# Kernel optimization log

Hardware: AMD Instinct MI355X
Metric: run time of the kernel (lower is better)

The kernel has to match this reference:

```python
import jax, jax.numpy as jnp
import numpy as np

NS, NV = 32, 8                      # scalar / vector multiplicities (32x0e + 8x1o)
N_NODES, N_EDGES = 16384, 131072
NEF, HID = 128, 128                 # edge feature dim, MLP hidden
WN = NS*NS + NV*NS + NS*NV + NV*NV  # 1600 tensor-product weights per edge
D = NS + 3*NV                       # 56 node feature dim
INV_SQRT3 = 1.0/np.sqrt(3.0)        # CG coeff for 1o x 1o -> 0e
PATH_NORM = 1.0/np.sqrt(NS + NV)    # fan-in normalization per output irrep
EPS = 1e-5


def setup_inputs() -> dict:
    key = jax.random.key(0)
    ks = jax.random.split(key, 10)
    node_attr = jax.random.normal(ks[0], (N_NODES, D), jnp.float32)
    edge_index = jax.random.randint(ks[1], (2, N_EDGES), 0, N_NODES, dtype=jnp.int64)
    edge_attr = jax.random.normal(ks[2], (N_EDGES, NEF), jnp.float32)
    edge_sh = jax.random.normal(ks[3], (N_EDGES, 4), jnp.float32)
    W1 = jax.random.normal(ks[4], (NEF, HID), jnp.float32) / np.sqrt(NEF)
    b1 = jnp.zeros((HID,), jnp.float32)
    W2 = jax.random.normal(ks[5], (HID, WN), jnp.float32) / np.sqrt(HID)
    b2 = jnp.zeros((WN,), jnp.float32)
    bn_gamma = jnp.ones((NS + NV,), jnp.float32)   # per-irrep scale (scalars then vectors)
    bn_beta = jnp.zeros((NS,), jnp.float32)        # bias only on scalar irreps
    return dict(node_attr=node_attr, edge_attr=edge_attr, edge_sh=edge_sh,
                W1=W1, b1=b1, W2=W2, b2=b2, bn_gamma=bn_gamma, bn_beta=bn_beta,
                edge_index=edge_index)


def reference(node_attr, edge_attr, edge_sh, W1, b1, W2, b2, bn_gamma, bn_beta, edge_index):
    edge_src, edge_dst = edge_index[0], edge_index[1]

    # per-edge tensor-product weights from edge MLP (dropout=0, eval mode)
    w = jax.nn.relu(edge_attr @ W1 + b1) @ W2 + b2            # [E, WN]
    o0 = NS*NS; o1 = o0 + NV*NS; o2 = o1 + NS*NV
    w_ss = w[:, :o0].reshape(-1, NS, NS)   # 0e x 0e -> 0e
    w_vs = w[:, o0:o1].reshape(-1, NV, NS) # 1o x 1o -> 0e
    w_sv = w[:, o1:o2].reshape(-1, NS, NV) # 0e x 1o -> 1o
    w_vv = w[:, o2:].reshape(-1, NV, NV)   # 1o x 0e -> 1o

    # gather node features onto edges
    x = node_attr[edge_dst]                # [E, D]
    xs = x[:, :NS]                         # [E, NS]
    xv = x[:, NS:].reshape(-1, NV, 3)      # [E, NV, 3]
    ss = edge_sh[:, 0]                     # [E]
    sv = edge_sh[:, 1:4]                   # [E, 3]

    # CG tensor product with per-edge fully-connected weights
    dot_vv = jnp.einsum('eim,em->ei', xv, sv) * INV_SQRT3
    out_s = (jnp.einsum('eij,ei->ej', w_ss, xs) * ss[:, None]
             + jnp.einsum('eij,ei->ej', w_vs, dot_vv)) * PATH_NORM          # [E, NS]
    out_v = (jnp.einsum('eij,ei->ej', w_sv, xs)[:, :, None] * sv[:, None, :]
             + jnp.einsum('eij,eim->ejm', w_vv, xv) * ss[:, None, None]) * PATH_NORM  # [E, NV, 3]
    tp = jnp.concatenate([out_s, out_v.reshape(-1, 3*NV)], axis=-1)         # [E, D]

    # scatter-mean to source nodes
    sums = jax.ops.segment_sum(tp, edge_src, num_segments=N_NODES)
    cnt = jax.ops.segment_sum(jnp.ones((tp.shape[0], 1), tp.dtype), edge_src,
                              num_segments=N_NODES)
    out = sums / jnp.maximum(cnt, 1.0)

    # residual (in/out irreps identical -> zero padding is a no-op)
    out = out + node_attr

    # equivariant batch norm (training-mode batch statistics)
    s = out[:, :NS]
    v = out[:, NS:].reshape(-1, NV, 3)
    s = (s - s.mean(0)) / jnp.sqrt(s.var(0) + EPS) * bn_gamma[:NS] + bn_beta
    vn2 = (v * v).sum(-1).mean(0)                               # [NV] mean squared norm
    v = v / jnp.sqrt(vn2 + EPS)[None, :, None] * bn_gamma[NS:][None, :, None]
    return jnp.concatenate([s, v.reshape(-1, 3*NV)], axis=-1)
```

## Files before the change

### kernel.cpp

```cpp
#include <hip/hip_runtime.h>

typedef short short8 __attribute__((ext_vector_type(8)));
typedef unsigned short us4 __attribute__((ext_vector_type(4)));
typedef float floatx4 __attribute__((ext_vector_type(4)));
typedef unsigned short u16;

#define NN 16384
#define NE 131072
#define NEF_ 128
#define DD 56
#define INV_SQRT3F 0.57735026918962576f
#define PATH_NORMF 0.15811388300841897f

__device__ __forceinline__ float bf2f(u16 u) {
    union { unsigned int i; float f; } v; v.i = ((unsigned int)u) << 16; return v.f;
}
__device__ __forceinline__ u16 f2bf(float f) {
    union { float f; unsigned int i; } v; v.f = f;
    unsigned int r = v.i + 0x7fffu + ((v.i >> 16) & 1u);
    return (u16)(r >> 16);
}

__global__ __launch_bounds__(256) void prep(const float* __restrict__ W1,
                                            const float* __restrict__ W2,
                                            u16* __restrict__ W1T,
                                            u16* __restrict__ W2T,
                                            const int* __restrict__ eidx,
                                            int* __restrict__ deg) {
    int b = blockIdx.x;
    if (b < 864) {
        int i = b * 256 + threadIdx.x;
        if (i < 16384) {
            int n = i >> 7, k = i & 127;
            W1T[i] = f2bf(W1[k * 128 + n]);
        } else {
            int j = i - 16384;
            int n = j >> 7, k = j & 127;
            W2T[j] = f2bf(W2[k * 1600 + n]);
        }
    } else {
        int e = (b - 864) * 256 + threadIdx.x;
        atomicAdd(&deg[eidx[e]], 1);
    }
}

__global__ __launch_bounds__(1024) void deg_scan(const int* __restrict__ deg,
                                                 int* __restrict__ row_start,
                                                 int* __restrict__ cursor) {
    __shared__ int part[1024];
    const int t = threadIdx.x;
    const int base = t * 16;
    int loc[16];
    int s = 0;
    #pragma unroll
    for (int i = 0; i < 16; i++) { loc[i] = s; s += deg[base + i]; }
    part[t] = s;
    __syncthreads();
    for (int off = 1; off < 1024; off <<= 1) {
        int v = (t >= off) ? part[t - off] : 0;
        __syncthreads();
        part[t] += v;
        __syncthreads();
    }
    int pre = (t == 0) ? 0 : part[t - 1];
    #pragma unroll
    for (int i = 0; i < 16; i++) {
        int v = pre + loc[i];
        row_start[base + i] = v;
        cursor[base + i] = v;
    }
    if (t == 1023) row_start[16384] = pre + s;
}

__global__ __launch_bounds__(256) void edge_scatter(const int* __restrict__ eidx,
                                                    int* __restrict__ cursor,
                                                    int* __restrict__ edge_order) {
    int e = blockIdx.x * 256 + threadIdx.x;
    int p = atomicAdd(&cursor[eidx[e]], 1);
    edge_order[p] = e;
}

__global__ __launch_bounds__(512, 4) void tpconv(
    const float* __restrict__ node_attr, const float* __restrict__ edge_attr,
    const float* __restrict__ edge_sh, const u16* __restrict__ W1T,
    const float* __restrict__ b1, const u16* __restrict__ W2T,
    const float* __restrict__ b2, const int* __restrict__ eidx,
    const int* __restrict__ edge_order,
    float* __restrict__ tp)
{
    __shared__ __align__(16) char smem[49920];
    u16*   sA  = (u16*)smem;
    u16*   sB  = (u16*)(smem + 17408);
    u16*   sF  = (u16*)(smem + 34816);
    float* b2s = (float*)(smem + 43520);
    float* Ssc  = (float*)smem;
    float* Svec = (float*)(smem + 16896);

    const int t = threadIdx.x;
    const int lane = t & 63;
    const int wv = t >> 6;
    const int m = lane & 15;
    const int q = lane >> 4;
    const int cg = wv & 3;
    const int eh = wv >> 2;
    const int eb = eh * 32;
    const int p0 = blockIdx.x * 64;
    const int str = t >> 4;
    const int stc = (t & 15) * 8;

    short8 pre[2];
    #pragma unroll
    for (int ii = 0; ii < 2; ii++)
        pre[ii] = *(const short8*)&W2T[(size_t)(str + 32 * ii) * 128 + stc];

    for (int i = t; i < 1600; i += 512) b2s[i] = b2[i];

    #pragma unroll
    for (int ii = 0; ii < 4; ii++) {
        int cid = t + 512 * ii;
        int r = cid >> 5, s = cid & 31;
        int e = edge_order[p0 + r];
        const float* src = &edge_attr[(size_t)e * NEF_ + s * 4];
        us4 o;
        o.x = f2bf(src[0]); o.y = f2bf(src[1]); o.z = f2bf(src[2]); o.w = f2bf(src[3]);
        *(us4*)&sA[r * 136 + s * 4] = o;
    }
    if (t < 64) {
        int e = edge_order[p0 + t];
        int nd = eidx[NE + e];
        const float* na = node_attr + (size_t)nd * DD;
        const float* sh = edge_sh + (size_t)e * 4;
        float ss = sh[0], s0 = sh[1], s1 = sh[2], s2 = sh[3];
        #pragma unroll
        for (int i = 0; i < 32; i++) sF[i * 64 + t] = f2bf(na[i]);
        #pragma unroll
        for (int i = 0; i < 8; i++) {
            float d = (na[32+i*3]*s0 + na[33+i*3]*s1 + na[34+i*3]*s2) * INV_SQRT3F;
            sF[(32 + i) * 64 + t] = f2bf(d);
        }
        #pragma unroll
        for (int i = 0; i < 24; i++) sF[(40 + i) * 64 + t] = f2bf(na[32 + i]);
        sF[64 * 64 + t] = f2bf(ss);
        sF[65 * 64 + t] = f2bf(s0);
        sF[66 * 64 + t] = f2bf(s1);
        sF[67 * 64 + t] = f2bf(s2);
    }
    __syncthreads();

    floatx4 hacc[2][2];
    #pragma unroll
    for (int cc = 0; cc < 2; cc++) {
        #pragma unroll
        for (int ii = 0; ii < 2; ii++)
            *(short8*)&sB[(str + 32 * ii) * 136 + stc] =
                *(const short8*)&W1T[(size_t)(cc * 64 + str + 32 * ii) * 128 + stc];
        __syncthreads();
        {
            float bv = b1[cc * 64 + cg * 16 + m];
            hacc[cc][0] = (floatx4){bv, bv, bv, bv};
            hacc[cc][1] = hacc[cc][0];
        }
        #pragma unroll
        for (int k0 = 0; k0 < 128; k0 += 32) {
            short8 a0 = *(const short8*)&sA[(eb      + m) * 136 + k0 + q * 8];
            short8 a1 = *(const short8*)&sA[(eb + 16 + m) * 136 + k0 + q * 8];
            short8 bA = *(const short8*)&sB[(cg * 16 + m) * 136 + k0 + q * 8];
            hacc[cc][0] = __builtin_amdgcn_mfma_f32_16x16x32_bf16(a0, bA, hacc[cc][0], 0, 0, 0);
            hacc[cc][1] = __builtin_amdgcn_mfma_f32_16x16x32_bf16(a1, bA, hacc[cc][1], 0, 0, 0);
        }
        __syncthreads();
    }
    #pragma unroll
    for (int cc = 0; cc < 2; cc++)
      #pragma unroll
      for (int rt = 0; rt < 2; rt++)
        #pragma unroll
        for (int r = 0; r < 4; r++) {
            int e   = eb + rt * 16 + q * 4 + r;
            int col = cc * 64 + cg * 16 + m;
            float v = hacc[cc][rt][r];
            sA[e * 136 + col] = f2bf(v > 0.f ? v : 0.f);
        }
    __syncthreads();

    short8 hc[2][4];
    #pragma unroll
    for (int et = 0; et < 2; et++)
        #pragma unroll
        for (int kk = 0; kk < 4; kk++)
            hc[et][kk] = *(const short8*)&sA[(eb + et * 16 + m) * 136 + kk * 32 + q * 8];

    float ssc[2], svc[2][3];
    #pragma unroll
    for (int et = 0; et < 2; et++) {
        ssc[et] = bf2f(sF[64 * 64 + eb + et * 16 + m]);
        svc[et][0] = bf2f(sF[65 * 64 + eb + et * 16 + m]);
        svc[et][1] = bf2f(sF[66 * 64 + eb + et * 16 + m]);
        svc[et][2] = bf2f(sF[67 * 64 + eb + et * 16 + m]);
    }

    #pragma unroll
    for (int ii = 0; ii < 2; ii++)
        *(short8*)&sB[(str + 32 * ii) * 136 + stc] = pre[ii];
    #pragma unroll
    for (int ii = 0; ii < 2; ii++)
        pre[ii] = *(const short8*)&W2T[(size_t)(64 + str + 32 * ii) * 128 + stc];
    __syncthreads();

    float tps[2][4];
    float tpv[2][4][3];
    #pragma unroll
    for (int et = 0; et < 2; et++)
        #pragma unroll
        for (int r = 0; r < 4; r++) {
            tps[et][r] = 0.f;
            tpv[et][r][0] = 0.f; tpv[et][r][1] = 0.f; tpv[et][r][2] = 0.f;
        }

    for (int c = 0; c < 25; c++) {
        floatx4 bias = *(const floatx4*)&b2s[c * 64 + cg * 16 + q * 4];
        floatx4 acc[2];
        acc[0] = bias; acc[1] = bias;
        #pragma unroll
        for (int kk = 0; kk < 4; kk++) {
            short8 a = *(const short8*)&sB[(cg * 16 + m) * 136 + kk * 32 + q * 8];
            acc[0] = __builtin_amdgcn_mfma_f32_16x16x32_bf16(a, hc[0][kk], acc[0], 0, 0, 0);
            acc[1] = __builtin_amdgcn_mfma_f32_16x16x32_bf16(a, hc[1][kk], acc[1], 0, 0, 0);
        }

        if (c < 16) {
            const int i = 2 * c + (cg >> 1);
            #pragma unroll
            for (int et = 0; et < 2; et++) {
                float f = bf2f(sF[i * 64 + eb + et * 16 + m]) * ssc[et];
                #pragma unroll
                for (int r = 0; r < 4; r++) tps[et][r] += acc[et][r] * f;
            }
        } else if (c < 20) {
            const int i = 2 * (c - 16) + (cg >> 1);
            #pragma unroll
            for (int et = 0; et < 2; et++) {
                float f = bf2f(sF[(32 + i) * 64 + eb + et * 16 + m]);
                #pragma unroll
                for (int r = 0; r < 4; r++) tps[et][r] += acc[et][r] * f;
            }
        } else if (c < 24) {
            const int i = 8 * (c - 20) + cg * 2 + (q >> 1);
            #pragma unroll
            for (int et = 0; et < 2; et++) {
                float f = bf2f(sF[i * 64 + eb + et * 16 + m]);
                #pragma unroll
                for (int r = 0; r < 4; r++) {
                    float t0 = acc[et][r] * f;
                    tpv[et][r][0] += t0 * svc[et][0];
                    tpv[et][r][1] += t0 * svc[et][1];
                    tpv[et][r][2] += t0 * svc[et][2];
                }
            }
        } else {
            const int i = cg * 2 + (q >> 1);
            #pragma unroll
            for (int et = 0; et < 2; et++) {
                float x0 = bf2f(sF[(40 + 3 * i + 0) * 64 + eb + et * 16 + m]) * ssc[et];
                float x1 = bf2f(sF[(40 + 3 * i + 1) * 64 + eb + et * 16 + m]) * ssc[et];
                float x2 = bf2f(sF[(40 + 3 * i + 2) * 64 + eb + et * 16 + m]) * ssc[et];
                #pragma unroll
                for (int r = 0; r < 4; r++) {
                    tpv[et][r][0] += acc[et][r] * x0;
                    tpv[et][r][1] += acc[et][r] * x1;
                    tpv[et][r][2] += acc[et][r] * x2;
                }
            }
        }

        __syncthreads();
        if (c < 24) {
            #pragma unroll
            for (int ii = 0; ii < 2; ii++)
                *(short8*)&sB[(str + 32 * ii) * 136 + stc] = pre[ii];
            if (c < 23) {
                #pragma unroll
                for (int ii = 0; ii < 2; ii++)
                    pre[ii] = *(const short8*)&W2T[(size_t)((c + 2) * 64 + str + 32 * ii) * 128 + stc];
            }
        }
        __syncthreads();
    }

    #pragma unroll
    for (int et = 0; et < 2; et++)
        #pragma unroll
        for (int r = 0; r < 4; r++)
            Ssc[(cg >> 1) * 2112 + (eb + et * 16 + m) * 33 + (cg & 1) * 16 + q * 4 + r] = tps[et][r];
    #pragma unroll
    for (int et = 0; et < 2; et++)
        #pragma unroll
        for (int r = 0; r < 4; r++)
            #pragma unroll
            for (int mm = 0; mm < 3; mm++) {
                float v = tpv[et][r][mm];
                v += __shfl_xor(v, 32, 64);
                if (q < 2)
                    Svec[cg * 1600 + (eb + et * 16 + m) * 25 + ((q & 1) * 4 + r) * 3 + mm] = v;
            }
    __syncthreads();

    for (int idx = t; idx < 3584; idx += 512) {
        int e = idx / 56, d = idx - e * 56;
        float v;
        if (d < 32) {
            v = Ssc[e * 33 + d] + Ssc[2112 + e * 33 + d];
        } else {
            int dd = d - 32;
            v = Svec[e * 25 + dd] + Svec[1600 + e * 25 + dd]
              + Svec[3200 + e * 25 + dd] + Svec[4800 + e * 25 + dd];
        }
        tp[(size_t)(p0 + e) * DD + d] = v * PATH_NORMF;
    }
}

__global__ __launch_bounds__(256) void gather_finalize(
    const float* __restrict__ tp, const int* __restrict__ row_start,
    const float* __restrict__ node_attr,
    float* __restrict__ ybuf, float* __restrict__ partial)
{
    __shared__ float ps[4][72];
    const int wv = threadIdx.x >> 6, lane = threadIdx.x & 63;
    const int n = blockIdx.x * 4 + wv;
    const int beg = row_start[n], end = row_start[n + 1];
    if (lane < 56) {
        float acc = 0.f;
        for (int p = beg; p < end; p++)
            acc += tp[(size_t)p * DD + lane];
        float inv = 1.f / fmaxf((float)(end - beg), 1.f);
        float y = acc * inv + node_attr[(size_t)n * DD + lane];
        ybuf[(size_t)n * DD + lane] = y;
        if (lane < 32) {
            ps[wv][lane] = y;
            ps[wv][32 + lane] = y * y;
        } else {
            float vv = y * y;
            float v1 = __shfl_down(vv, 1, 64);
            float v2 = __shfl_down(vv, 2, 64);
            int l3 = lane - 32;
            if (l3 % 3 == 0) ps[wv][64 + l3 / 3] = vv + v1 + v2;
        }
    }
    __syncthreads();
    const int t = threadIdx.x;
    if (t < 72)
        partial[(size_t)blockIdx.x * 72 + t] = ps[0][t] + ps[1][t] + ps[2][t] + ps[3][t];
}

__global__ __launch_bounds__(256) void bn_reduce(const float* __restrict__ partial,
                                                 float* __restrict__ stats)
{
    __shared__ float red[256];
    const int d = blockIdx.x;
    const int t = threadIdx.x;
    float a = 0.f;
    for (int i = t; i < 4096; i += 256) a += partial[(size_t)i * 72 + d];
    red[t] = a;
    __syncthreads();
    for (int off = 128; off > 0; off >>= 1) {
        if (t < off) red[t] += red[t + off];
        __syncthreads();
    }
    if (t == 0) stats[d] = red[0] * (1.f / 16384.f);
}

__global__ __launch_bounds__(256) void bn_apply(
    const float* __restrict__ ybuf, const float* __restrict__ stats,
    const float* __restrict__ gamma, const float* __restrict__ beta,
    float* __restrict__ out)
{
    const int i = blockIdx.x * 256 + threadIdx.x;
    const int n = i / 56;
    const int d = i - n * 56;
    float y = ybuf[i];
    float o;
    if (d < 32) {
        float mn  = stats[d];
        float var = stats[32 + d] - mn * mn;
        o = (y - mn) * rsqrtf(var + 1e-5f) * gamma[d] + beta[d];
    } else {
        int jv = (d - 32) / 3;
        o = y * rsqrtf(stats[64 + jv] + 1e-5f) * gamma[32 + jv];
    }
    out[i] = o;
}

extern "C" void kernel_launch(void* const* d_in, const int* in_sizes, int n_in,
                              void* d_out, int out_size, void* d_ws, size_t ws_size,
                              hipStream_t stream)
{
    const float* node_attr = (const float*)d_in[0];
    const float* edge_attr = (const float*)d_in[1];
    const float* edge_sh   = (const float*)d_in[2];
    const float* W1        = (const float*)d_in[3];
    const float* b1        = (const float*)d_in[4];
    const float* W2        = (const float*)d_in[5];
    const float* b2        = (const float*)d_in[6];
    const float* gamma     = (const float*)d_in[7];
    const float* beta      = (const float*)d_in[8];
    const int*   eidx      = (const int*)d_in[9];

    char* ws = (char*)d_ws;
    u16*   W1T        = (u16*)(ws);
    u16*   W2T        = (u16*)(ws + 32768);
    int*   deg        = (int*)(ws + 442368);
    int*   row_start  = (int*)(ws + 507904);
    int*   cursor     = (int*)(ws + 573696);
    int*   edge_order = (int*)(ws + 639232);
    float* stats      = (float*)(ws + 1163520);
    float* partial    = (float*)(ws + 1164032);
    float* tp         = (float*)(ws + 2343680);
    float* ybuf       = (float*)(ws + 31703808);

    (void)hipMemsetAsync(deg, 0, 65536, stream);
    hipLaunchKernelGGL(prep,            dim3(1376), dim3(256),  0, stream,
                       W1, W2, W1T, W2T, eidx, deg);
    hipLaunchKernelGGL(deg_scan,        dim3(1),    dim3(1024), 0, stream, deg, row_start, cursor);
    hipLaunchKernelGGL(edge_scatter,    dim3(512),  dim3(256),  0, stream, eidx, cursor, edge_order);
    hipLaunchKernelGGL(tpconv,          dim3(2048), dim3(512),  0, stream,
                       node_attr, edge_attr, edge_sh, W1T, b1, W2T, b2, eidx, edge_order, tp);
    hipLaunchKernelGGL(gather_finalize, dim3(4096), dim3(256),  0, stream,
                       tp, row_start, node_attr, ybuf, partial);
    hipLaunchKernelGGL(bn_reduce,       dim3(72),   dim3(256),  0, stream, partial, stats);
    hipLaunchKernelGGL(bn_apply,        dim3(3584), dim3(256),  0, stream,
                       ybuf, stats, gamma, beta, (float*)d_out);
}
```

Measured before the change: 256.2 us.

## Load W2 MFMA fragments directly from global and fold BN reduce into atomics

The tensor-product kernel no longer stages W2 chunks through shared memory with two block barriers per chunk. Each wave now loads its MFMA A-fragments straight from global (L2-resident) memory into registers, double-buffered two chunks ahead, and the chunk loop is split by irrep path to drop the branch. Separately, the per-block BN partial sums are accumulated with float atomics into a zeroed stats buffer, which removes the bn_reduce kernel. The trade is more register pressure and redundant global loads per wave, plus nondeterministic float summation order in the statistics.

Result: slower. 491.5 us (+91.8%).

```diff
diff --git a/kernel.cpp b/kernel.cpp
--- a/kernel.cpp
+++ b/kernel.cpp
@@ -80,6 +80,61 @@
     edge_order[p] = e;
 }
 
+#define CHUNK_MFMA(FA, C)                                                        \
+    floatx4 acc[2];                                                              \
+    {                                                                            \
+        floatx4 bias = *(const floatx4*)&b2s[(C) * 64 + cg * 16 + q * 4];        \
+        acc[0] = bias; acc[1] = bias;                                            \
+        _Pragma("unroll")                                                        \
+        for (int kk = 0; kk < 4; kk++) {                                         \
+            acc[0] = __builtin_amdgcn_mfma_f32_16x16x32_bf16(FA[kk], hc[0][kk], acc[0], 0, 0, 0); \
+            acc[1] = __builtin_amdgcn_mfma_f32_16x16x32_bf16(FA[kk], hc[1][kk], acc[1], 0, 0, 0); \
+        }                                                                        \
+    }
+
+#define PREFETCH_G(FA, C)                                                        \
+    _Pragma("unroll")                                                            \
+    for (int kk = 0; kk < 4; kk++)                                               \
+        FA[kk] = *(const short8*)(wfrag + (size_t)(C) * 8192 + kk * 32);
+
+#define CONSUME_SS(C)                                                            \
+    {                                                                            \
+        const int i = 2 * (C) + (cg >> 1);                                       \
+        _Pragma("unroll")                                                        \
+        for (int et = 0; et < 2; et++) {                                         \
+            float f = bf2f(sF[i * 64 + eb + et * 16 + m]) * ssc[et];             \
+            _Pragma("unroll")                                                    \
+            for (int r = 0; r < 4; r++) tps[et][r] += acc[et][r] * f;            \
+        }                                                                        \
+    }
+
+#define CONSUME_VS(C)                                                            \
+    {                                                                            \
+        const int i = 2 * ((C) - 16) + (cg >> 1);                                \
+        _Pragma("unroll")                                                        \
+        for (int et = 0; et < 2; et++) {                                         \
+            float f = bf2f(sF[(32 + i) * 64 + eb + et * 16 + m]);                \
+            _Pragma("unroll")                                                    \
+            for (int r = 0; r < 4; r++) tps[et][r] += acc[et][r] * f;            \
+        }                                                                        \
+    }
+
+#define CONSUME_SV(C)                                                            \
+    {                                                                            \
+        const int i = 8 * ((C) - 20) + cg * 2 + (q >> 1);                        \
+        _Pragma("unroll")                                                        \
+        for (int et = 0; et < 2; et++) {                                         \
+            float f = bf2f(sF[i * 64 + eb + et * 16 + m]);                       \
+            _Pragma("unroll")                                                    \
+            for (int r = 0; r < 4; r++) {                                        \
+                float t0 = acc[et][r] * f;                                       \
+                tpv[et][r][0] += t0 * svc[et][0];                                \
+                tpv[et][r][1] += t0 * svc[et][1];                                \
+                tpv[et][r][2] += t0 * svc[et][2];                                \
+            }                                                                    \
+        }                                                                        \
+    }
+
 __global__ __launch_bounds__(512, 4) void tpconv(
     const float* __restrict__ node_attr, const float* __restrict__ edge_attr,
     const float* __restrict__ edge_sh, const u16* __restrict__ W1T,
@@ -108,10 +163,10 @@
     const int str = t >> 4;
     const int stc = (t & 15) * 8;
 
-    short8 pre[2];
-    #pragma unroll
-    for (int ii = 0; ii < 2; ii++)
-        pre[ii] = *(const short8*)&W2T[(size_t)(str + 32 * ii) * 128 + stc];
+    const u16* wfrag = W2T + (size_t)(cg * 16 + m) * 128 + q * 8;
+    short8 fa0[4], fa1[4];
+    PREFETCH_G(fa0, 0)
+    PREFETCH_G(fa1, 1)
 
     for (int i = t; i < 1600; i += 512) b2s[i] = b2[i];
 
@@ -199,14 +254,6 @@
         svc[et][2] = bf2f(sF[67 * 64 + eb + et * 16 + m]);
     }
 
-    #pragma unroll
-    for (int ii = 0; ii < 2; ii++)
-        *(short8*)&sB[(str + 32 * ii) * 136 + stc] = pre[ii];
-    #pragma unroll
-    for (int ii = 0; ii < 2; ii++)
-        pre[ii] = *(const short8*)&W2T[(size_t)(64 + str + 32 * ii) * 128 + stc];
-    __syncthreads();
-
     float tps[2][4];
     float tpv[2][4][3];
     #pragma unroll
@@ -217,75 +264,42 @@
             tpv[et][r][0] = 0.f; tpv[et][r][1] = 0.f; tpv[et][r][2] = 0.f;
         }
 
-    for (int c = 0; c < 25; c++) {
-        floatx4 bias = *(const floatx4*)&b2s[c * 64 + cg * 16 + q * 4];
-        floatx4 acc[2];
-        acc[0] = bias; acc[1] = bias;
-        #pragma unroll
-        for (int kk = 0; kk < 4; kk++) {
-            short8 a = *(const short8*)&sB[(cg * 16 + m) * 136 + kk * 32 + q * 8];
-            acc[0] = __builtin_amdgcn_mfma_f32_16x16x32_bf16(a, hc[0][kk], acc[0], 0, 0, 0);
-            acc[1] = __builtin_amdgcn_mfma_f32_16x16x32_bf16(a, hc[1][kk], acc[1], 0, 0, 0);
-        }
-
-        if (c < 16) {
-            const int i = 2 * c + (cg >> 1);
+    #pragma unroll 1
+    for (int c = 0; c < 16; c += 2) {
+        { CHUNK_MFMA(fa0, c)     PREFETCH_G(fa0, c + 2) CONSUME_SS(c) }
+        { CHUNK_MFMA(fa1, c + 1) PREFETCH_G(fa1, c + 3) CONSUME_SS(c + 1) }
+    }
+    #pragma unroll 1
+    for (int c = 16; c < 20; c += 2) {
+        { CHUNK_MFMA(fa0, c)     PREFETCH_G(fa0, c + 2) CONSUME_VS(c) }
+        { CHUNK_MFMA(fa1, c + 1) PREFETCH_G(fa1, c + 3) CONSUME_VS(c + 1) }
+    }
+    #pragma unroll 1
+    for (int c = 20; c < 24; c += 2) {
+        { CHUNK_MFMA(fa0, c)     PREFETCH_G(fa0, c + 2) CONSUME_SV(c) }
+        {
+            CHUNK_MFMA(fa1, c + 1)
+            if (c + 3 < 25) { PREFETCH_G(fa1, c + 3) }
+            CONSUME_SV(c + 1)
+        }
+    }
+    {
+        CHUNK_MFMA(fa0, 24)
+        const int i = cg * 2 + (q >> 1);
+        #pragma unroll
+        for (int et = 0; et < 2; et++) {
+            float x0 = bf2f(sF[(40 + 3 * i + 0) * 64 + eb + et * 16 + m]) * ssc[et];
+            float x1 = bf2f(sF[(40 + 3 * i + 1) * 64 + eb + et * 16 + m]) * ssc[et];
+            float x2 = bf2f(sF[(40 + 3 * i + 2) * 64 + eb + et * 16 + m]) * ssc[et];
             #pragma unroll
-            for (int et = 0; et < 2; et++) {
-                float f = bf2f(sF[i * 64 + eb + et * 16 + m]) * ssc[et];
-                #pragma unroll
-                for (int r = 0; r < 4; r++) tps[et][r] += acc[et][r] * f;
+            for (int r = 0; r < 4; r++) {
+                tpv[et][r][0] += acc[et][r] * x0;
+                tpv[et][r][1] += acc[et][r] * x1;
+                tpv[et][r][2] += acc[et][r] * x2;
             }
-        } else if (c < 20) {
-            const int i = 2 * (c - 16) + (cg >> 1);
-            #pragma unroll
-            for (int et = 0; et < 2; et++) {
-                float f = bf2f(sF[(32 + i) * 64 + eb + et * 16 + m]);
-                #pragma unroll
-                for (int r = 0; r < 4; r++) tps[et][r] += acc[et][r] * f;
-            }
-        } else if (c < 24) {
-            const int i = 8 * (c - 20) + cg * 2 + (q >> 1);
-            #pragma unroll
-            for (int et = 0; et < 2; et++) {
-                float f = bf2f(sF[i * 64 + eb + et * 16 + m]);
-                #pragma unroll
-                for (int r = 0; r < 4; r++) {
-                    float t0 = acc[et][r] * f;
-                    tpv[et][r][0] += t0 * svc[et][0];
-                    tpv[et][r][1] += t0 * svc[et][1];
-                    tpv[et][r][2] += t0 * svc[et][2];
-                }
-            }
-        } else {
-            const int i = cg * 2 + (q >> 1);
-            #pragma unroll
-            for (int et = 0; et < 2; et++) {
-                float x0 = bf2f(sF[(40 + 3 * i + 0) * 64 + eb + et * 16 + m]) * ssc[et];
-                float x1 = bf2f(sF[(40 + 3 * i + 1) * 64 + eb + et * 16 + m]) * ssc[et];
-                float x2 = bf2f(sF[(40 + 3 * i + 2) * 64 + eb + et * 16 + m]) * ssc[et];
-                #pragma unroll
-                for (int r = 0; r < 4; r++) {
-                    tpv[et][r][0] += acc[et][r] * x0;
-                    tpv[et][r][1] += acc[et][r] * x1;
-                    tpv[et][r][2] += acc[et][r] * x2;
-                }
-            }
-        }
-
-        __syncthreads();
-        if (c < 24) {
-            #pragma unroll
-            for (int ii = 0; ii < 2; ii++)
-                *(short8*)&sB[(str + 32 * ii) * 136 + stc] = pre[ii];
-            if (c < 23) {
-                #pragma unroll
-                for (int ii = 0; ii < 2; ii++)
-                    pre[ii] = *(const short8*)&W2T[(size_t)((c + 2) * 64 + str + 32 * ii) * 128 + stc];
-            }
-        }
-        __syncthreads();
-    }
+        }
+    }
+    __syncthreads();
 
     #pragma unroll
     for (int et = 0; et < 2; et++)
@@ -322,7 +336,7 @@
 __global__ __launch_bounds__(256) void gather_finalize(
     const float* __restrict__ tp, const int* __restrict__ row_start,
     const float* __restrict__ node_attr,
-    float* __restrict__ ybuf, float* __restrict__ partial)
+    float* __restrict__ ybuf, float* __restrict__ stats)
 {
     __shared__ float ps[4][72];
     const int wv = threadIdx.x >> 6, lane = threadIdx.x & 63;
@@ -349,24 +363,7 @@
     __syncthreads();
     const int t = threadIdx.x;
     if (t < 72)
-        partial[(size_t)blockIdx.x * 72 + t] = ps[0][t] + ps[1][t] + ps[2][t] + ps[3][t];
-}
-
-__global__ __launch_bounds__(256) void bn_reduce(const float* __restrict__ partial,
-                                                 float* __restrict__ stats)
-{
-    __shared__ float red[256];
-    const int d = blockIdx.x;
-    const int t = threadIdx.x;
-    float a = 0.f;
-    for (int i = t; i < 4096; i += 256) a += partial[(size_t)i * 72 + d];
-    red[t] = a;
-    __syncthreads();
-    for (int off = 128; off > 0; off >>= 1) {
-        if (t < off) red[t] += red[t + off];
-        __syncthreads();
-    }
-    if (t == 0) stats[d] = red[0] * (1.f / 16384.f);
+        atomicAdd(&stats[t], ps[0][t] + ps[1][t] + ps[2][t] + ps[3][t]);
 }
 
 __global__ __launch_bounds__(256) void bn_apply(
@@ -377,15 +374,16 @@
     const int i = blockIdx.x * 256 + threadIdx.x;
     const int n = i / 56;
     const int d = i - n * 56;
+    const float invN = 1.f / 16384.f;
     float y = ybuf[i];
     float o;
     if (d < 32) {
-        float mn  = stats[d];
-        float var = stats[32 + d] - mn * mn;
+        float mn  = stats[d] * invN;
+        float var = stats[32 + d] * invN - mn * mn;
         o = (y - mn) * rsqrtf(var + 1e-5f) * gamma[d] + beta[d];
     } else {
         int jv = (d - 32) / 3;
-        o = y * rsqrtf(stats[64 + jv] + 1e-5f) * gamma[32 + jv];
+        o = y * rsqrtf(stats[64 + jv] * invN + 1e-5f) * gamma[32 + jv];
     }
     out[i] = o;
 }
@@ -409,15 +407,14 @@
     u16*   W1T        = (u16*)(ws);
     u16*   W2T        = (u16*)(ws + 32768);
     int*   deg        = (int*)(ws + 442368);
-    int*   row_start  = (int*)(ws + 507904);
-    int*   cursor     = (int*)(ws + 573696);
-    int*   edge_order = (int*)(ws + 639232);
-    float* stats      = (float*)(ws + 1163520);
-    float* partial    = (float*)(ws + 1164032);
-    float* tp         = (float*)(ws + 2343680);
-    float* ybuf       = (float*)(ws + 31703808);
-
-    (void)hipMemsetAsync(deg, 0, 65536, stream);
+    float* stats      = (float*)(ws + 507904);
+    int*   row_start  = (int*)(ws + 508416);
+    int*   cursor     = (int*)(ws + 574208);
+    int*   edge_order = (int*)(ws + 639744);
+    float* tp         = (float*)(ws + 1164032);
+    float* ybuf       = (float*)(ws + 30524160);
+
+    (void)hipMemsetAsync(deg, 0, 66048, stream);
     hipLaunchKernelGGL(prep,            dim3(1376), dim3(256),  0, stream,
                        W1, W2, W1T, W2T, eidx, deg);
     hipLaunchKernelGGL(deg_scan,        dim3(1),    dim3(1024), 0, stream, deg, row_start, cursor);
@@ -425,8 +422,7 @@
     hipLaunchKernelGGL(tpconv,          dim3(2048), dim3(512),  0, stream,
                        node_attr, edge_attr, edge_sh, W1T, b1, W2T, b2, eidx, edge_order, tp);
     hipLaunchKernelGGL(gather_finalize, dim3(4096), dim3(256),  0, stream,
-                       tp, row_start, node_attr, ybuf, partial);
-    hipLaunchKernelGGL(bn_reduce,       dim3(72),   dim3(256),  0, stream, partial, stats);
+                       tp, row_start, node_attr, ybuf, stats);
     hipLaunchKernelGGL(bn_apply,        dim3(3584), dim3(256),  0, stream,
                        ybuf, stats, gamma, beta, (float*)d_out);
 }
```

## Pre-swizzle weights into MFMA fragment order and fold BN reduce into atomics

Applied to the files above, without the earlier changes.

The prep kernel now writes W1 and W2 in bf16, already arranged in the per-lane MFMA fragment order. Staging them in shared memory becomes a contiguous, unpadded copy, and each lane reads its B operand with one linear 16-byte load instead of a padded strided one. This saves a little LDS and removes address math and bank conflicts. Separately, the bn_reduce kernel and its partials buffer are removed: gather_finalize atomically adds block sums into a stats array zeroed by the existing memset, and bn_apply scales by 1/N. The atomics on 72 addresses from 4096 blocks may contend, and float atomic ordering makes the sums nondeterministic.

Result: slower. 334.3 us (+30.5%).

```diff
diff --git a/kernel.cpp b/kernel.cpp
--- a/kernel.cpp
+++ b/kernel.cpp
@@ -23,20 +23,24 @@
 
 __global__ __launch_bounds__(256) void prep(const float* __restrict__ W1,
                                             const float* __restrict__ W2,
-                                            u16* __restrict__ W1T,
-                                            u16* __restrict__ W2T,
+                                            u16* __restrict__ W1f,
+                                            u16* __restrict__ W2f,
                                             const int* __restrict__ eidx,
                                             int* __restrict__ deg) {
     int b = blockIdx.x;
     if (b < 864) {
         int i = b * 256 + threadIdx.x;
         if (i < 16384) {
-            int n = i >> 7, k = i & 127;
-            W1T[i] = f2bf(W1[k * 128 + n]);
+            int cc = i >> 13, kk = (i >> 11) & 3, cg = (i >> 9) & 3;
+            int lane = (i >> 3) & 63, j = i & 7;
+            int q = lane >> 4, m = lane & 15;
+            W1f[i] = f2bf(W1[(kk * 32 + q * 8 + j) * 128 + cc * 64 + cg * 16 + m]);
         } else {
-            int j = i - 16384;
-            int n = j >> 7, k = j & 127;
-            W2T[j] = f2bf(W2[k * 1600 + n]);
+            int f = i - 16384;
+            int c = f >> 13, kk = (f >> 11) & 3, cg = (f >> 9) & 3;
+            int lane = (f >> 3) & 63, j = f & 7;
+            int q = lane >> 4, m = lane & 15;
+            W2f[f] = f2bf(W2[(kk * 32 + q * 8 + j) * 1600 + c * 64 + cg * 16 + m]);
         }
     } else {
         int e = (b - 864) * 256 + threadIdx.x;
@@ -82,17 +86,17 @@
 
 __global__ __launch_bounds__(512, 4) void tpconv(
     const float* __restrict__ node_attr, const float* __restrict__ edge_attr,
-    const float* __restrict__ edge_sh, const u16* __restrict__ W1T,
-    const float* __restrict__ b1, const u16* __restrict__ W2T,
+    const float* __restrict__ edge_sh, const u16* __restrict__ W1f,
+    const float* __restrict__ b1, const u16* __restrict__ W2f,
     const float* __restrict__ b2, const int* __restrict__ eidx,
     const int* __restrict__ edge_order,
     float* __restrict__ tp)
 {
-    __shared__ __align__(16) char smem[49920];
+    __shared__ __align__(16) char smem[48896];
     u16*   sA  = (u16*)smem;
-    u16*   sB  = (u16*)(smem + 17408);
-    u16*   sF  = (u16*)(smem + 34816);
-    float* b2s = (float*)(smem + 43520);
+    u16*   B2  = (u16*)(smem + 17408);
+    u16*   sF  = (u16*)(smem + 33792);
+    float* b2s = (float*)(smem + 42496);
     float* Ssc  = (float*)smem;
     float* Svec = (float*)(smem + 16896);
 
@@ -105,13 +109,11 @@
     const int eh = wv >> 2;
     const int eb = eh * 32;
     const int p0 = blockIdx.x * 64;
-    const int str = t >> 4;
-    const int stc = (t & 15) * 8;
 
     short8 pre[2];
     #pragma unroll
     for (int ii = 0; ii < 2; ii++)
-        pre[ii] = *(const short8*)&W2T[(size_t)(str + 32 * ii) * 128 + stc];
+        pre[ii] = *(const short8*)&W2f[ii * 4096 + t * 8];
 
     for (int i = t; i < 1600; i += 512) b2s[i] = b2[i];
 
@@ -152,8 +154,8 @@
     for (int cc = 0; cc < 2; cc++) {
         #pragma unroll
         for (int ii = 0; ii < 2; ii++)
-            *(short8*)&sB[(str + 32 * ii) * 136 + stc] =
-                *(const short8*)&W1T[(size_t)(cc * 64 + str + 32 * ii) * 128 + stc];
+            *(short8*)&B2[ii * 4096 + t * 8] =
+                *(const short8*)&W1f[cc * 8192 + ii * 4096 + t * 8];
         __syncthreads();
         {
             float bv = b1[cc * 64 + cg * 16 + m];
@@ -161,10 +163,10 @@
             hacc[cc][1] = hacc[cc][0];
         }
         #pragma unroll
-        for (int k0 = 0; k0 < 128; k0 += 32) {
-            short8 a0 = *(const short8*)&sA[(eb      + m) * 136 + k0 + q * 8];
-            short8 a1 = *(const short8*)&sA[(eb + 16 + m) * 136 + k0 + q * 8];
-            short8 bA = *(const short8*)&sB[(cg * 16 + m) * 136 + k0 + q * 8];
+        for (int kk = 0; kk < 4; kk++) {
+            short8 a0 = *(const short8*)&sA[(eb      + m) * 136 + kk * 32 + q * 8];
+            short8 a1 = *(const short8*)&sA[(eb + 16 + m) * 136 + kk * 32 + q * 8];
+            short8 bA = *(const short8*)&B2[(kk * 4 + cg) * 512 + lane * 8];
             hacc[cc][0] = __builtin_amdgcn_mfma_f32_16x16x32_bf16(a0, bA, hacc[cc][0], 0, 0, 0);
             hacc[cc][1] = __builtin_amdgcn_mfma_f32_16x16x32_bf16(a1, bA, hacc[cc][1], 0, 0, 0);
         }
@@ -201,10 +203,10 @@
 
     #pragma unroll
     for (int ii = 0; ii < 2; ii++)
-        *(short8*)&sB[(str + 32 * ii) * 136 + stc] = pre[ii];
+        *(short8*)&B2[ii * 4096 + t * 8] = pre[ii];
     #pragma unroll
     for (int ii = 0; ii < 2; ii++)
-        pre[ii] = *(const short8*)&W2T[(size_t)(64 + str + 32 * ii) * 128 + stc];
+        pre[ii] = *(const short8*)&W2f[8192 + ii * 4096 + t * 8];
     __syncthreads();
 
     float tps[2][4];
@@ -223,7 +225,7 @@
         acc[0] = bias; acc[1] = bias;
         #pragma unroll
         for (int kk = 0; kk < 4; kk++) {
-            short8 a = *(const short8*)&sB[(cg * 16 + m) * 136 + kk * 32 + q * 8];
+            short8 a = *(const short8*)&B2[(kk * 4 + cg) * 512 + lane * 8];
             acc[0] = __builtin_amdgcn_mfma_f32_16x16x32_bf16(a, hc[0][kk], acc[0], 0, 0, 0);
             acc[1] = __builtin_amdgcn_mfma_f32_16x16x32_bf16(a, hc[1][kk], acc[1], 0, 0, 0);
         }
@@ -277,11 +279,11 @@
         if (c < 24) {
             #pragma unroll
             for (int ii = 0; ii < 2; ii++)
-                *(short8*)&sB[(str + 32 * ii) * 136 + stc] = pre[ii];
+                *(short8*)&B2[ii * 4096 + t * 8] = pre[ii];
             if (c < 23) {
                 #pragma unroll
                 for (int ii = 0; ii < 2; ii++)
-                    pre[ii] = *(const short8*)&W2T[(size_t)((c + 2) * 64 + str + 32 * ii) * 128 + stc];
+                    pre[ii] = *(const short8*)&W2f[(size_t)(c + 2) * 8192 + ii * 4096 + t * 8];
             }
         }
         __syncthreads();
@@ -322,7 +324,7 @@
 __global__ __launch_bounds__(256) void gather_finalize(
     const float* __restrict__ tp, const int* __restrict__ row_start,
     const float* __restrict__ node_attr,
-    float* __restrict__ ybuf, float* __restrict__ partial)
+    float* __restrict__ ybuf, float* __restrict__ stats)
 {
     __shared__ float ps[4][72];
     const int wv = threadIdx.x >> 6, lane = threadIdx.x & 63;
@@ -349,24 +351,7 @@
     __syncthreads();
     const int t = threadIdx.x;
     if (t < 72)
-        partial[(size_t)blockIdx.x * 72 + t] = ps[0][t] + ps[1][t] + ps[2][t] + ps[3][t];
-}
-
-__global__ __launch_bounds__(256) void bn_reduce(const float* __restrict__ partial,
-                                                 float* __restrict__ stats)
-{
-    __shared__ float red[256];
-    const int d = blockIdx.x;
-    const int t = threadIdx.x;
-    float a = 0.f;
-    for (int i = t; i < 4096; i += 256) a += partial[(size_t)i * 72 + d];
-    red[t] = a;
-    __syncthreads();
-    for (int off = 128; off > 0; off >>= 1) {
-        if (t < off) red[t] += red[t + off];
-        __syncthreads();
-    }
-    if (t == 0) stats[d] = red[0] * (1.f / 16384.f);
+        atomicAdd(&stats[t], ps[0][t] + ps[1][t] + ps[2][t] + ps[3][t]);
 }
 
 __global__ __launch_bounds__(256) void bn_apply(
@@ -377,15 +362,16 @@
     const int i = blockIdx.x * 256 + threadIdx.x;
     const int n = i / 56;
     const int d = i - n * 56;
+    const float invN = 1.f / 16384.f;
     float y = ybuf[i];
     float o;
     if (d < 32) {
-        float mn  = stats[d];
-        float var = stats[32 + d] - mn * mn;
+        float mn  = stats[d] * invN;
+        float var = stats[32 + d] * invN - mn * mn;
         o = (y - mn) * rsqrtf(var + 1e-5f) * gamma[d] + beta[d];
     } else {
         int jv = (d - 32) / 3;
-        o = y * rsqrtf(stats[64 + jv] + 1e-5f) * gamma[32 + jv];
+        o = y * rsqrtf(stats[64 + jv] * invN + 1e-5f) * gamma[32 + jv];
     }
     out[i] = o;
 }
@@ -406,27 +392,25 @@
     const int*   eidx      = (const int*)d_in[9];
 
     char* ws = (char*)d_ws;
-    u16*   W1T        = (u16*)(ws);
-    u16*   W2T        = (u16*)(ws + 32768);
+    u16*   W1f        = (u16*)(ws);
+    u16*   W2f        = (u16*)(ws + 32768);
     int*   deg        = (int*)(ws + 442368);
-    int*   row_start  = (int*)(ws + 507904);
-    int*   cursor     = (int*)(ws + 573696);
-    int*   edge_order = (int*)(ws + 639232);
-    float* stats      = (float*)(ws + 1163520);
-    float* partial    = (float*)(ws + 1164032);
-    float* tp         = (float*)(ws + 2343680);
-    float* ybuf       = (float*)(ws + 31703808);
-
-    (void)hipMemsetAsync(deg, 0, 65536, stream);
+    float* stats      = (float*)(ws + 507904);
+    int*   row_start  = (int*)(ws + 508416);
+    int*   cursor     = (int*)(ws + 574208);
+    int*   edge_order = (int*)(ws + 639744);
+    float* tp         = (float*)(ws + 1164032);
+    float* ybuf       = (float*)(ws + 30524160);
+
+    (void)hipMemsetAsync(deg, 0, 66048, stream);
     hipLaunchKernelGGL(prep,            dim3(1376), dim3(256),  0, stream,
-                       W1, W2, W1T, W2T, eidx, deg);
+                       W1, W2, W1f, W2f, eidx, deg);
     hipLaunchKernelGGL(deg_scan,        dim3(1),    dim3(1024), 0, stream, deg, row_start, cursor);
     hipLaunchKernelGGL(edge_scatter,    dim3(512),  dim3(256),  0, stream, eidx, cursor, edge_order);
     hipLaunchKernelGGL(tpconv,          dim3(2048), dim3(512),  0, stream,
-                       node_attr, edge_attr, edge_sh, W1T, b1, W2T, b2, eidx, edge_order, tp);
+                       node_attr, edge_attr, edge_sh, W1f, b1, W2f, b2, eidx, edge_order, tp);
     hipLaunchKernelGGL(gather_finalize, dim3(4096), dim3(256),  0, stream,
-                       tp, row_start, node_attr, ybuf, partial);
-    hipLaunchKernelGGL(bn_reduce,       dim3(72),   dim3(256),  0, stream, partial, stats);
+                       tp, row_start, node_attr, ybuf, stats);
     hipLaunchKernelGGL(bn_apply,        dim3(3584), dim3(256),  0, stream,
                        ybuf, stats, gamma, beta, (float*)d_out);
 }
```
